# Performance work log

Measured on AMD Instinct MI355X. Metric: run time of the kernel, lower is better.

The kernel has to match this reference:

```python
import jax, jax.numpy as jnp
import numpy as np

HEADS = 8
DEPTH = 2
LN_EPS = 1e-5


def _layernorm(x, g, b):
    m = jnp.mean(x, axis=-1, keepdims=True)
    v = jnp.var(x, axis=-1, keepdims=True)
    return (x - m) / jnp.sqrt(v + LN_EPS) * g + b


def setup_inputs() -> dict:
    key = jax.random.key(0)
    ks = jax.random.split(key, 16)
    b, c, n, t = 4, 64, 512, 12
    L, H = DEPTH, 256  # depth, mlp_dim
    s = 0.05
    return {
        'x': jax.random.normal(ks[0], (b, c, n, t), jnp.float32),
        'adj': jax.random.uniform(ks[1], (n, n), jnp.float32) / n,
        'pos': 0.02 * jax.random.normal(ks[2], (1, n, c), jnp.float32),
        'qkv_w': s * jax.random.normal(ks[3], (L, 3 * c, c), jnp.float32),
        'proj_w': s * jax.random.normal(ks[4], (L, c, c), jnp.float32),
        'proj_b': jnp.zeros((L, c), jnp.float32),
        'ln_g': jnp.ones((L, c), jnp.float32),
        'ln_b': jnp.zeros((L, c), jnp.float32),
        'ff_w1': s * jax.random.normal(ks[5], (L, H, c), jnp.float32),
        'ff_b1': jnp.zeros((L, H), jnp.float32),
        'ff_w2': s * jax.random.normal(ks[6], (L, c, H), jnp.float32),
        'ff_b2': jnp.zeros((L, c), jnp.float32),
        'gcn_w': s * jax.random.normal(ks[7], (L, c, 3 * c), jnp.float32),  # Conv2d 1x1: [c_out, 3*c_in]
        'gcn_b': jnp.zeros((L, c), jnp.float32),
    }


def reference(x, adj, pos, qkv_w, proj_w, proj_b, ln_g, ln_b,
              ff_w1, ff_b1, ff_w2, ff_b2, gcn_w, gcn_b):
    b, c, n, t = x.shape
    hd = c // HEADS
    scale = hd ** (-0.5)
    # [b, c, n, t] -> [b*t, n, c]
    h = jnp.transpose(x, (0, 3, 2, 1)).reshape(b * t, n, c) + pos
    for l in range(DEPTH):
        residual = h.reshape(b, t, n, c)
        # --- manual MHA (no pre-norm around attention, faithful to source) ---
        qkv = jnp.einsum('bnc,oc->bno', h, qkv_w[l])  # [bt, n, 3c]
        qkv = qkv.reshape(b * t, n, 3, HEADS, hd).transpose(2, 0, 3, 1, 4)
        q, k, v = qkv[0], qkv[1], qkv[2]  # [bt, heads, n, hd]
        attn = jax.nn.softmax(jnp.einsum('bhnd,bhmd->bhnm', q, k) * scale, axis=-1)
        o = jnp.einsum('bhnm,bhmd->bhnd', attn, v)
        o = o.transpose(0, 2, 1, 3).reshape(b * t, n, c)
        o = jnp.einsum('bnc,oc->bno', o, proj_w[l]) + proj_b[l]
        h = o + h
        # --- PreNorm FeedForward ---
        y = _layernorm(h, ln_g[l], ln_b[l])
        y = jax.nn.gelu(jnp.einsum('bnc,hc->bnh', y, ff_w1[l]) + ff_b1[l], approximate=False)
        y = jnp.einsum('bnh,ch->bnc', y, ff_w2[l]) + ff_b2[l]
        h = y + h
        # --- GCN on residual (order=2 diffusion) ---
        r = jnp.transpose(residual, (0, 3, 2, 1))  # [b, c, n, t]
        x1 = jnp.einsum('bcvt,vw->bcwt', r, adj)
        x2 = jnp.einsum('bcvt,vw->bcwt', x1, adj)
        cat = jnp.concatenate([r, x1, x2], axis=1)  # [b, 3c, n, t]
        g = jnp.einsum('bknt,ok->bont', cat, gcn_w[l]) + gcn_b[l][None, :, None, None]
        h = jnp.transpose(g, (0, 3, 2, 1)).reshape(b * t, n, c) + h
    return jnp.transpose(h.reshape(b, t, n, c), (0, 3, 2, 1))
```

## Files before the change

### kernel.cpp

```cpp
#include <hip/hip_runtime.h>
#include <math.h>


typedef __fp16 half_t;
typedef __attribute__((ext_vector_type(2))) __fp16 half2v;
typedef __attribute__((ext_vector_type(4))) __fp16 half4v;
typedef __attribute__((ext_vector_type(4))) float f32x4;

union PU  { half2v h2[2]; half4v h4; };
union F4H { float4 f; half4v h[2]; };
union F2H { float2 f2; half4v h4; };

__global__ __launch_bounds__(256) void k_init(const float* __restrict__ x,
                                              const float* __restrict__ pos,
                                              float* __restrict__ h) {
    int i = blockIdx.x * 256 + threadIdx.x;
    int c = i & 63;
    int v = (i >> 6) & 511;
    int bt = i >> 15;
    int b = bt / 12, t = bt - b * 12;
    h[i] = x[(((size_t)(b * 64 + c) * 512) + v) * 12 + t] + pos[v * 64 + c];
}

__global__ __launch_bounds__(256) void k_prep(const float* __restrict__ qkv_w,
                                              const float* __restrict__ proj_w,
                                              const float* __restrict__ ff_w1,
                                              const float* __restrict__ ff_w2,
                                              const float* __restrict__ gcn_w,
                                              half_t* __restrict__ dst) {
    int i = blockIdx.x * 256 + threadIdx.x;
    float v;
    if (i < 24576) v = qkv_w[i];
    else if (i < 32768) v = proj_w[i - 24576];
    else if (i < 65536) v = ff_w1[i - 32768];
    else if (i < 98304) v = ff_w2[i - 65536];
    else v = gcn_w[i - 98304];
    dst[i] = (half_t)v;
}

__global__ __launch_bounds__(256) void k_adjt(const float* __restrict__ adj,
                                              half_t* __restrict__ adjTh) {
    __shared__ float t[64 * 65];
    int tid = threadIdx.x;
    int v0 = blockIdx.x * 64, w0 = blockIdx.y * 64;
#pragma unroll
    for (int i = 0; i < 4; ++i) {
        int g = tid + i * 256;
        int r = g >> 4, q = g & 15;
        float4 a = *(const float4*)(adj + (size_t)(v0 + r) * 512 + w0 + 4 * q);
        t[(4 * q + 0) * 65 + r] = a.x;
        t[(4 * q + 1) * 65 + r] = a.y;
        t[(4 * q + 2) * 65 + r] = a.z;
        t[(4 * q + 3) * 65 + r] = a.w;
    }
    __syncthreads();
#pragma unroll
    for (int i = 0; i < 4; ++i) {
        int g = tid + i * 256;
        int rw = g >> 4, q = g & 15;
        const float* src = &t[rw * 65 + 4 * q];
        PU u;
        u.h2[0] = __builtin_amdgcn_cvt_pkrtz(src[0], src[1]);
        u.h2[1] = __builtin_amdgcn_cvt_pkrtz(src[2], src[3]);
        *(half4v*)(adjTh + (size_t)(w0 + rw) * 512 + v0 + 4 * q) = u.h4;
    }
}

#define ATS 72
#define BTS 68

__global__ __launch_bounds__(256) void k_adj2(const half_t* __restrict__ adjTh,
                                              half_t* __restrict__ adjT2h) {
    __shared__ half_t a_t[64 * ATS];
    __shared__ half_t b_t[64 * BTS];
    int tid = threadIdx.x;
    int wave = tid >> 6, lane = tid & 63;
    int lm = lane & 15, lg = lane >> 4;
    int w0 = blockIdx.x * 64, v0 = blockIdx.y * 64;
    const f32x4 zc = {0.f, 0.f, 0.f, 0.f};
    f32x4 acc[4] = {zc, zc, zc, zc};

    for (int kc = 0; kc < 8; ++kc) {
#pragma unroll
        for (int i = 0; i < 2; ++i) {
            int g = tid + i * 256;
            int r = g >> 3, s = g & 7;
            *(float4*)&a_t[r * ATS + s * 8] =
                *(const float4*)(adjTh + (size_t)(w0 + r) * 512 + kc * 64 + s * 8);
        }
#pragma unroll
        for (int i = 0; i < 2; ++i) {
            int g = tid + i * 256;
            int ur = g >> 3, s = g & 7;
            F4H u;
            u.f = *(const float4*)(adjTh + (size_t)(kc * 64 + ur) * 512 + v0 + s * 8);
#pragma unroll
            for (int e = 0; e < 8; ++e)
                b_t[(s * 8 + e) * BTS + ur] = u.h[e >> 2][e & 3];
        }
        __syncthreads();
#pragma unroll
        for (int k16 = 0; k16 < 4; ++k16) {
            half4v af = *(const half4v*)&a_t[(wave * 16 + lm) * ATS + k16 * 16 + lg * 4];
#pragma unroll
            for (int nt = 0; nt < 4; ++nt) {
                half4v bf = *(const half4v*)&b_t[(nt * 16 + lm) * BTS + k16 * 16 + lg * 4];
                acc[nt] = __builtin_amdgcn_mfma_f32_16x16x16f16(af, bf, acc[nt], 0, 0, 0);
            }
        }
        __syncthreads();
    }
#pragma unroll
    for (int nt = 0; nt < 4; ++nt)
#pragma unroll
        for (int r = 0; r < 4; ++r)
            adjT2h[(size_t)(w0 + wave * 16 + lg * 4 + r) * 512 + v0 + nt * 16 + lm] =
                (half_t)acc[nt][r];
}

__global__ __launch_bounds__(128) void k_qkv(const float* __restrict__ h,
                                             const half_t* __restrict__ Wh,
                                             half_t* __restrict__ qh,
                                             half_t* __restrict__ kh,
                                             half_t* __restrict__ vh) {
    int wid = blockIdx.x * 2 + (threadIdx.x >> 6);
    int lane = threadIdx.x & 63;
    int lm = lane & 15, lg = lane >> 4;
    int row = wid * 16 + lm;

    half4v xf[4];
#pragma unroll
    for (int kc = 0; kc < 4; ++kc) {
        float4 a = *(const float4*)(h + (size_t)row * 64 + kc * 16 + lg * 4);
        PU u;
        u.h2[0] = __builtin_amdgcn_cvt_pkrtz(a.x, a.y);
        u.h2[1] = __builtin_amdgcn_cvt_pkrtz(a.z, a.w);
        xf[kc] = u.h4;
    }

    const f32x4 zc = {0.f, 0.f, 0.f, 0.f};
    const float SC = 0.35355339059327373f * 1.4426950408889634f;
    int bt = row >> 9, v = row & 511;

    half4v wf[4];
#pragma unroll
    for (int kc = 0; kc < 4; ++kc)
        wf[kc] = *(const half4v*)(Wh + (size_t)lm * 64 + kc * 16 + lg * 4);

#pragma unroll
    for (int nt = 0; nt < 12; ++nt) {
        half4v cw[4];
#pragma unroll
        for (int kc = 0; kc < 4; ++kc) cw[kc] = wf[kc];
        if (nt < 11) {
#pragma unroll
            for (int kc = 0; kc < 4; ++kc)
                wf[kc] = *(const half4v*)(Wh + (size_t)((nt + 1) * 16 + lm) * 64 + kc * 16 + lg * 4);
        }
        f32x4 acc = zc;
#pragma unroll
        for (int kc = 0; kc < 4; ++kc)
            acc = __builtin_amdgcn_mfma_f32_16x16x16f16(cw[kc], xf[kc], acc, 0, 0, 0);
        int s = nt >> 2;
        if (s == 0) { acc[0] *= SC; acc[1] *= SC; acc[2] *= SC; acc[3] *= SC; }
        int head = ((nt & 3) << 1) + (lg >> 1);
        int d0 = (lg & 1) * 4;
        PU o2;
        o2.h2[0] = __builtin_amdgcn_cvt_pkrtz(acc[0], acc[1]);
        o2.h2[1] = __builtin_amdgcn_cvt_pkrtz(acc[2], acc[3]);
        half_t* dst = (s == 0) ? qh : ((s == 1) ? kh : vh);
        *(half4v*)(dst + ((size_t)(bt * 8 + head) * 512 + v) * 8 + d0) = o2.h4;
    }
}

#define KLS 20
#define QLS 20
#define VTS 516

__global__ __launch_bounds__(512) void k_attn(const half_t* __restrict__ qh,
                                              const half_t* __restrict__ kh,
                                              const half_t* __restrict__ vh,
                                              half_t* __restrict__ obh) {
    __shared__ half_t kl[512 * KLS];
    __shared__ half_t vt[16 * VTS];
    __shared__ half_t ql[256 * QLS];
    int bh = blockIdx.x >> 1;
    int half_ = blockIdx.x & 1;
    int tid = threadIdx.x;
    const half_t* kbase = kh + (size_t)bh * 4096;
    const half_t* vbase = vh + (size_t)bh * 4096;
    const half_t* qbase = qh + (size_t)bh * 4096 + half_ * 2048;
    const half4v zero4 = {(__fp16)0.f, (__fp16)0.f, (__fp16)0.f, (__fp16)0.f};

    if (tid < 256) {
#pragma unroll
        for (int kk = 0; kk < 2; ++kk) {
            int key = tid * 2 + kk;
            F4H u;
            u.f = *(const float4*)(kbase + key * 8);
            half4v* rowp = (half4v*)&kl[key * KLS];
            rowp[0] = u.h[0];
            rowp[1] = u.h[1];
            rowp[2] = zero4;
            rowp[3] = zero4;
        }
        {
            F4H u;
            u.f = *(const float4*)(qbase + tid * 8);
            half4v* rowp = (half4v*)&ql[tid * QLS];
            rowp[0] = u.h[0];
            rowp[1] = u.h[1];
            rowp[2] = zero4;
            rowp[3] = zero4;
        }
        {
            int k0 = tid * 2;
            F4H a, b;
            a.f = *(const float4*)(vbase + k0 * 8);
            b.f = *(const float4*)(vbase + k0 * 8 + 8);
#pragma unroll
            for (int d = 0; d < 8; ++d) {
                half2v p = {a.h[d >> 2][d & 3], b.h[d >> 2][d & 3]};
                *(half2v*)&vt[d * VTS + k0] = p;
            }
        }
    }
    for (int i = tid; i < 1032; i += 512)
        ((half4v*)(vt + 8 * VTS))[i] = zero4;
    __syncthreads();

    int wave = tid >> 6, lane = tid & 63;
    int lm = lane & 15, lg = lane >> 4;
    int bt = bh >> 3, head = bh & 7;

#pragma unroll 1
    for (int st = 0; st < 2; ++st) {
        int qrow0 = wave * 32 + st * 16;
        half4v qf = *(const half4v*)&ql[(qrow0 + lm) * QLS + lg * 4];
        f32x4 acc = {0.f, 0.f, 0.f, 0.f};
        float l0 = 0.f, l1 = 0.f, l2 = 0.f, l3 = 0.f;
        f32x4 zc = {0.f, 0.f, 0.f, 0.f};
#pragma unroll 4
        for (int kt = 0; kt < 32; ++kt) {
            int key0 = kt * 16;
            half4v ka = *(const half4v*)&kl[(key0 + lm) * KLS + lg * 4];
            f32x4 c1 = __builtin_amdgcn_mfma_f32_16x16x16f16(ka, qf, zc, 0, 0, 0);
            float p0 = exp2f(fminf(c1[0], 12.f));
            float p1 = exp2f(fminf(c1[1], 12.f));
            float p2 = exp2f(fminf(c1[2], 12.f));
            float p3 = exp2f(fminf(c1[3], 12.f));
            l0 += p0; l1 += p1; l2 += p2; l3 += p3;
            PU pu;
            pu.h2[0] = __builtin_amdgcn_cvt_pkrtz(p0, p1);
            pu.h2[1] = __builtin_amdgcn_cvt_pkrtz(p2, p3);
            half4v va = *(const half4v*)&vt[lm * VTS + key0 + lg * 4];
            acc = __builtin_amdgcn_mfma_f32_16x16x16f16(va, pu.h4, acc, 0, 0, 0);
        }
        float lsum = (l0 + l1) + (l2 + l3);
        lsum += __shfl_xor(lsum, 16);
        lsum += __shfl_xor(lsum, 32);
        if (lg < 2) {
            float inv = 1.f / lsum;
            int rowg = half_ * 256 + qrow0 + lm;
            PU o2;
            o2.h2[0] = __builtin_amdgcn_cvt_pkrtz(acc[0] * inv, acc[1] * inv);
            o2.h2[1] = __builtin_amdgcn_cvt_pkrtz(acc[2] * inv, acc[3] * inv);
            *(half4v*)(obh + ((size_t)(bt * 512 + rowg)) * 64 + head * 8 + lg * 4) = o2.h4;
        }
    }
}

__global__ __launch_bounds__(256) void k_diffx2(const half_t* __restrict__ adjTh,
                                                const half_t* __restrict__ adjT2h,
                                                const float* __restrict__ h,
                                                half_t* __restrict__ x1h,
                                                half_t* __restrict__ x2h) {
    __shared__ half_t a_t[64 * ATS];
    __shared__ half_t b_t[64 * BTS];
    int tid = threadIdx.x;
    int wave = tid >> 6, lane = tid & 63;
    int lm = lane & 15, lg = lane >> 4;
    int w0 = blockIdx.x * 64;
    int bt = blockIdx.y;
    const half_t* A = blockIdx.z ? adjT2h : adjTh;
    half_t* outb = blockIdx.z ? x2h : x1h;
    const f32x4 zc = {0.f, 0.f, 0.f, 0.f};
    f32x4 acc[4] = {zc, zc, zc, zc};

    for (int kc = 0; kc < 8; ++kc) {
#pragma unroll
        for (int i = 0; i < 2; ++i) {
            int g = tid + i * 256;
            int r = g >> 3, s = g & 7;
            *(float4*)&a_t[r * ATS + s * 8] =
                *(const float4*)(A + (size_t)(w0 + r) * 512 + kc * 64 + s * 8);
        }
#pragma unroll
        for (int i = 0; i < 4; ++i) {
            int g = tid + i * 256;
            int vr = g >> 4, q = g & 15;
            float4 a = *(const float4*)(h + ((size_t)(bt * 512 + kc * 64 + vr)) * 64 + 4 * q);
            b_t[(4 * q + 0) * BTS + vr] = (half_t)a.x;
            b_t[(4 * q + 1) * BTS + vr] = (half_t)a.y;
            b_t[(4 * q + 2) * BTS + vr] = (half_t)a.z;
            b_t[(4 * q + 3) * BTS + vr] = (half_t)a.w;
        }
        __syncthreads();
#pragma unroll
        for (int k16 = 0; k16 < 4; ++k16) {
            half4v af = *(const half4v*)&a_t[(wave * 16 + lm) * ATS + k16 * 16 + lg * 4];
#pragma unroll
            for (int nt = 0; nt < 4; ++nt) {
                half4v bf = *(const half4v*)&b_t[(nt * 16 + lm) * BTS + k16 * 16 + lg * 4];
                acc[nt] = __builtin_amdgcn_mfma_f32_16x16x16f16(af, bf, acc[nt], 0, 0, 0);
            }
        }
        __syncthreads();
    }
#pragma unroll
    for (int nt = 0; nt < 4; ++nt)
#pragma unroll
        for (int r = 0; r < 4; ++r)
            outb[(size_t)(w0 + wave * 16 + lg * 4 + r) * 3072 + bt * 64 + nt * 16 + lm] =
                (half_t)acc[nt][r];
}

__global__ __launch_bounds__(256) void k_gcn(const float* __restrict__ h,
                                             const half_t* __restrict__ x1h,
                                             const half_t* __restrict__ x2h,
                                             const half_t* __restrict__ Wh,
                                             const float* __restrict__ bias,
                                             float* __restrict__ gout) {
    __shared__ half_t a_t[64 * ATS];
    __shared__ half_t b_t[64 * BTS];
    int tid = threadIdx.x;
    int wave = tid >> 6, lane = tid & 63;
    int lm = lane & 15, lg = lane >> 4;
    int row0 = blockIdx.x * 64;
    const f32x4 zc = {0.f, 0.f, 0.f, 0.f};
    f32x4 acc[4] = {zc, zc, zc, zc};

    for (int ch = 0; ch < 3; ++ch) {
        if (ch == 0) {
#pragma unroll
            for (int i = 0; i < 4; ++i) {
                int g = tid + i * 256;
                int r = g >> 4, q = g & 15;
                int rowg = row0 + r;
                int v = rowg / 48, bt = rowg - v * 48;
                float4 a = *(const float4*)(h + ((size_t)(bt * 512 + v)) * 64 + 4 * q);
                PU ua;
                ua.h2[0] = __builtin_amdgcn_cvt_pkrtz(a.x, a.y);
                ua.h2[1] = __builtin_amdgcn_cvt_pkrtz(a.z, a.w);
                *(half4v*)&a_t[r * ATS + 4 * q] = ua.h4;
            }
        } else {
            const half_t* X = (ch == 1) ? x1h : x2h;
#pragma unroll
            for (int i = 0; i < 2; ++i) {
                int g = tid + i * 256;
                int r = g >> 3, s = g & 7;
                *(float4*)&a_t[r * ATS + s * 8] =
                    *(const float4*)(X + (size_t)(row0 + r) * 64 + s * 8);
            }
        }
#pragma unroll
        for (int i = 0; i < 4; ++i) {
            int g = tid + i * 256;
            int r = g >> 4, q = g & 15;
            *(half4v*)&b_t[r * BTS + 4 * q] =
                *(const half4v*)(Wh + (size_t)r * 192 + ch * 64 + 4 * q);
        }
        __syncthreads();
#pragma unroll
        for (int k16 = 0; k16 < 4; ++k16) {
            half4v af = *(const half4v*)&a_t[(wave * 16 + lm) * ATS + k16 * 16 + lg * 4];
#pragma unroll
            for (int nt = 0; nt < 4; ++nt) {
                half4v bf = *(const half4v*)&b_t[(nt * 16 + lm) * BTS + k16 * 16 + lg * 4];
                acc[nt] = __builtin_amdgcn_mfma_f32_16x16x16f16(bf, af, acc[nt], 0, 0, 0);
            }
        }
        __syncthreads();
    }
    int row = row0 + wave * 16 + lm;
    int v = row / 48, bt = row - v * 48;
    float* gp = gout + ((size_t)(bt * 512 + v)) * 64;
#pragma unroll
    for (int nt = 0; nt < 4; ++nt) {
        float4 bb = *(const float4*)(bias + nt * 16 + lg * 4);
        *(float4*)(gp + nt * 16 + lg * 4) =
            make_float4(acc[nt][0] + bb.x, acc[nt][1] + bb.y,
                        acc[nt][2] + bb.z, acc[nt][3] + bb.w);
    }
}

__global__ __launch_bounds__(128) void k_plf(const half_t* __restrict__ obh,
                                             const half_t* __restrict__ pwh,
                                             const float* __restrict__ pb,
                                             const float* __restrict__ g,
                                             const float* __restrict__ bln,
                                             const half_t* __restrict__ w1h,
                                             const float* __restrict__ b1,
                                             const half_t* __restrict__ w2h,
                                             const float* __restrict__ b2,
                                             const float* __restrict__ gout,
                                             float* __restrict__ h) {
    int wid = blockIdx.x * 2 + (threadIdx.x >> 6);
    int lane = threadIdx.x & 63;
    int lm = lane & 15, lg = lane >> 4;
    int row = wid * 16 + lm;
    const f32x4 zc = {0.f, 0.f, 0.f, 0.f};

    half4v pf[4];
#pragma unroll
    for (int kc = 0; kc < 4; ++kc)
        pf[kc] = *(const half4v*)(pwh + (size_t)lm * 64 + kc * 16 + lg * 4);

    half4v of[4];
#pragma unroll
    for (int kc = 0; kc < 4; ++kc) {
        F2H u;
        u.f2 = *(const float2*)(obh + (size_t)row * 64 + kc * 16 + lg * 4);
        of[kc] = u.h4;
    }

    f32x4 hp[4];
#pragma unroll
    for (int nt = 0; nt < 4; ++nt) {
        half4v cw[4];
#pragma unroll
        for (int kc = 0; kc < 4; ++kc) cw[kc] = pf[kc];
        if (nt < 3) {
#pragma unroll
            for (int kc = 0; kc < 4; ++kc)
                pf[kc] = *(const half4v*)(pwh + (size_t)((nt + 1) * 16 + lm) * 64 + kc * 16 + lg * 4);
        }
        f32x4 c = zc;
#pragma unroll
        for (int kc = 0; kc < 4; ++kc)
            c = __builtin_amdgcn_mfma_f32_16x16x16f16(cw[kc], of[kc], c, 0, 0, 0);
        float4 ho = *(const float4*)(h + (size_t)row * 64 + nt * 16 + lg * 4);
        float4 bb = *(const float4*)(pb + nt * 16 + lg * 4);
        hp[nt][0] = c[0] + ho.x + bb.x;
        hp[nt][1] = c[1] + ho.y + bb.y;
        hp[nt][2] = c[2] + ho.z + bb.z;
        hp[nt][3] = c[3] + ho.w + bb.w;
    }

    float s = 0.f, s2 = 0.f;
#pragma unroll
    for (int nt = 0; nt < 4; ++nt)
#pragma unroll
        for (int r = 0; r < 4; ++r) {
            s += hp[nt][r];
            s2 += hp[nt][r] * hp[nt][r];
        }
    s += __shfl_xor(s, 16);  s2 += __shfl_xor(s2, 16);
    s += __shfl_xor(s, 32);  s2 += __shfl_xor(s2, 32);
    float mean = s * (1.f / 64.f);
    float var = s2 * (1.f / 64.f) - mean * mean;
    float rstd = rsqrtf(var + 1e-5f);

    half4v xf[4];
#pragma unroll
    for (int nt = 0; nt < 4; ++nt) {
        float4 gg = *(const float4*)(g + nt * 16 + lg * 4);
        float4 bb = *(const float4*)(bln + nt * 16 + lg * 4);
        float y0 = (hp[nt][0] - mean) * rstd * gg.x + bb.x;
        float y1 = (hp[nt][1] - mean) * rstd * gg.y + bb.y;
        float y2 = (hp[nt][2] - mean) * rstd * gg.z + bb.z;
        float y3 = (hp[nt][3] - mean) * rstd * gg.w + bb.w;
        PU u;
        u.h2[0] = __builtin_amdgcn_cvt_pkrtz(y0, y1);
        u.h2[1] = __builtin_amdgcn_cvt_pkrtz(y2, y3);
        xf[nt] = u.h4;
    }

    half4v w1f[4];
#pragma unroll
    for (int kc = 0; kc < 4; ++kc)
        w1f[kc] = *(const half4v*)(w1h + (size_t)lm * 64 + kc * 16 + lg * 4);

    f32x4 acc[4] = {zc, zc, zc, zc};
#pragma unroll 4
    for (int ht = 0; ht < 16; ++ht) {
        half4v cw[4];
#pragma unroll
        for (int kc = 0; kc < 4; ++kc) cw[kc] = w1f[kc];
        half4v w2f[4];
#pragma unroll
        for (int ot = 0; ot < 4; ++ot)
            w2f[ot] = *(const half4v*)(w2h + (size_t)(ot * 16 + lm) * 256 + ht * 16 + lg * 4);
        if (ht < 15) {
#pragma unroll
            for (int kc = 0; kc < 4; ++kc)
                w1f[kc] = *(const half4v*)(w1h + (size_t)((ht + 1) * 16 + lm) * 64 + kc * 16 + lg * 4);
        }
        f32x4 c1 = zc;
#pragma unroll
        for (int kc = 0; kc < 4; ++kc)
            c1 = __builtin_amdgcn_mfma_f32_16x16x16f16(cw[kc], xf[kc], c1, 0, 0, 0);
        float4 bb = *(const float4*)(b1 + ht * 16 + lg * 4);
        float y0 = c1[0] + bb.x;
        float y1 = c1[1] + bb.y;
        float y2 = c1[2] + bb.z;
        float y3 = c1[3] + bb.w;
        y0 = 0.5f * y0 * (1.0f + erff(y0 * 0.70710678118654752f));
        y1 = 0.5f * y1 * (1.0f + erff(y1 * 0.70710678118654752f));
        y2 = 0.5f * y2 * (1.0f + erff(y2 * 0.70710678118654752f));
        y3 = 0.5f * y3 * (1.0f + erff(y3 * 0.70710678118654752f));
        PU p;
        p.h2[0] = __builtin_amdgcn_cvt_pkrtz(y0, y1);
        p.h2[1] = __builtin_amdgcn_cvt_pkrtz(y2, y3);
#pragma unroll
        for (int ot = 0; ot < 4; ++ot)
            acc[ot] = __builtin_amdgcn_mfma_f32_16x16x16f16(w2f[ot], p.h4, acc[ot], 0, 0, 0);
    }

#pragma unroll
    for (int ot = 0; ot < 4; ++ot) {
        float4 bb = *(const float4*)(b2 + ot * 16 + lg * 4);
        float4 gv = *(const float4*)(gout + (size_t)row * 64 + ot * 16 + lg * 4);
        *(float4*)(h + (size_t)row * 64 + ot * 16 + lg * 4) =
            make_float4(hp[ot][0] + acc[ot][0] + bb.x + gv.x,
                        hp[ot][1] + acc[ot][1] + bb.y + gv.y,
                        hp[ot][2] + acc[ot][2] + bb.z + gv.z,
                        hp[ot][3] + acc[ot][3] + bb.w + gv.w);
    }
}

__global__ __launch_bounds__(256) void k_out(const float* __restrict__ h,
                                             float* __restrict__ out) {
    int i = blockIdx.x * 256 + threadIdx.x;
    int t = i % 12;
    int r = i / 12;
    int v = r & 511;
    int r2 = r >> 9;
    int c = r2 & 63;
    int b = r2 >> 6;
    out[i] = h[(((size_t)(b * 12 + t) * 512) + v) * 64 + c];
}

extern "C" void kernel_launch(void* const* d_in, const int* in_sizes, int n_in,
                              void* d_out, int out_size, void* d_ws, size_t ws_size,
                              hipStream_t stream) {
    const float* x      = (const float*)d_in[0];
    const float* adj    = (const float*)d_in[1];
    const float* pos    = (const float*)d_in[2];
    const float* qkv_w  = (const float*)d_in[3];
    const float* proj_w = (const float*)d_in[4];
    const float* proj_b = (const float*)d_in[5];
    const float* ln_g   = (const float*)d_in[6];
    const float* ln_b   = (const float*)d_in[7];
    const float* ff_w1  = (const float*)d_in[8];
    const float* ff_b1  = (const float*)d_in[9];
    const float* ff_w2  = (const float*)d_in[10];
    const float* ff_b2  = (const float*)d_in[11];
    const float* gcn_w  = (const float*)d_in[12];
    const float* gcn_b  = (const float*)d_in[13];
    float* out = (float*)d_out;

    const size_t SZ = 1572864;
    float* h    = (float*)d_ws;
    float* gout = h + SZ;
    half_t* x1h = (half_t*)(gout + SZ);
    half_t* x2h = x1h + SZ;
    half_t* qh  = x2h + SZ;
    half_t* kh  = qh + SZ;
    half_t* vh  = kh + SZ;
    half_t* obh = vh + SZ;
    half_t* adjTh  = obh + SZ;
    half_t* adjT2h = adjTh + 262144;
    half_t* wh     = adjT2h + 262144;
    half_t* qkv_wh  = wh;
    half_t* proj_wh = wh + 24576;
    half_t* ff_w1h  = wh + 32768;
    half_t* ff_w2h  = wh + 65536;
    half_t* gcn_wh  = wh + 98304;

    k_init<<<6144, 256, 0, stream>>>(x, pos, h);
    k_adjt<<<dim3(8, 8), 256, 0, stream>>>(adj, adjTh);
    k_prep<<<480, 256, 0, stream>>>(qkv_w, proj_w, ff_w1, ff_w2, gcn_w, wh);
    k_adj2<<<dim3(8, 8), 256, 0, stream>>>(adjTh, adjT2h);
    for (int l = 0; l < 2; ++l) {
        k_qkv<<<768, 128, 0, stream>>>(h, qkv_wh + l * 12288, qh, kh, vh);
        k_attn<<<768, 512, 0, stream>>>(qh, kh, vh, obh);
        k_diffx2<<<dim3(8, 48, 2), 256, 0, stream>>>(adjTh, adjT2h, h, x1h, x2h);
        k_gcn<<<384, 256, 0, stream>>>(h, x1h, x2h, gcn_wh + l * 12288, gcn_b + l * 64, gout);
        k_plf<<<768, 128, 0, stream>>>(obh, proj_wh + l * 4096, proj_b + l * 64,
                                       ln_g + l * 64, ln_b + l * 64,
                                       ff_w1h + l * 16384, ff_b1 + l * 256,
                                       ff_w2h + l * 16384, ff_b2 + l * 64, gout, h);
    }
    k_out<<<6144, 256, 0, stream>>>(h, out);
}
```

Baseline: 320.6 us.

## Merge independent kernels via block-index dispatch and tile init/out transposes

Merges the prep kernels (input transpose, adj transpose, weight conversion) into one launch, runs QKV projection together with the adjacency diffusion in one launch, and runs attention together with the GCN channel mix in another, each role picked by block index. Independent stages can then overlap on the GPU and there are fewer launches per layer. The init and output permutes now go through shared-memory tiles so global accesses coalesce. The cost is heterogeneous blocks: the GCN part runs at 512 threads with half of them idle, and the fused kernels must size their shared memory for the larger role.

```diff
diff --git a/kernel.cpp b/kernel.cpp
--- a/kernel.cpp
+++ b/kernel.cpp
@@ -11,63 +11,85 @@
 union F4H { float4 f; half4v h[2]; };
 union F2H { float2 f2; half4v h4; };
 
-__global__ __launch_bounds__(256) void k_init(const float* __restrict__ x,
-                                              const float* __restrict__ pos,
-                                              float* __restrict__ h) {
-    int i = blockIdx.x * 256 + threadIdx.x;
-    int c = i & 63;
-    int v = (i >> 6) & 511;
-    int bt = i >> 15;
-    int b = bt / 12, t = bt - b * 12;
-    h[i] = x[(((size_t)(b * 64 + c) * 512) + v) * 12 + t] + pos[v * 64 + c];
-}
-
-__global__ __launch_bounds__(256) void k_prep(const float* __restrict__ qkv_w,
-                                              const float* __restrict__ proj_w,
-                                              const float* __restrict__ ff_w1,
-                                              const float* __restrict__ ff_w2,
-                                              const float* __restrict__ gcn_w,
-                                              half_t* __restrict__ dst) {
-    int i = blockIdx.x * 256 + threadIdx.x;
-    float v;
-    if (i < 24576) v = qkv_w[i];
-    else if (i < 32768) v = proj_w[i - 24576];
-    else if (i < 65536) v = ff_w1[i - 32768];
-    else if (i < 98304) v = ff_w2[i - 65536];
-    else v = gcn_w[i - 98304];
-    dst[i] = (half_t)v;
-}
-
-__global__ __launch_bounds__(256) void k_adjt(const float* __restrict__ adj,
-                                              half_t* __restrict__ adjTh) {
+#define ATS 72
+#define BTS 68
+#define KLS 20
+#define QLS 20
+#define VTS 516
+
+__global__ __launch_bounds__(256) void k_pre(const float* __restrict__ x,
+                                             const float* __restrict__ pos,
+                                             const float* __restrict__ adj,
+                                             const float* __restrict__ qkv_w,
+                                             const float* __restrict__ proj_w,
+                                             const float* __restrict__ ff_w1,
+                                             const float* __restrict__ ff_w2,
+                                             const float* __restrict__ gcn_w,
+                                             float* __restrict__ h,
+                                             half_t* __restrict__ adjTh,
+                                             half_t* __restrict__ wh) {
     __shared__ float t[64 * 65];
     int tid = threadIdx.x;
-    int v0 = blockIdx.x * 64, w0 = blockIdx.y * 64;
-#pragma unroll
-    for (int i = 0; i < 4; ++i) {
-        int g = tid + i * 256;
-        int r = g >> 4, q = g & 15;
-        float4 a = *(const float4*)(adj + (size_t)(v0 + r) * 512 + w0 + 4 * q);
-        t[(4 * q + 0) * 65 + r] = a.x;
-        t[(4 * q + 1) * 65 + r] = a.y;
-        t[(4 * q + 2) * 65 + r] = a.z;
-        t[(4 * q + 3) * 65 + r] = a.w;
-    }
-    __syncthreads();
-#pragma unroll
-    for (int i = 0; i < 4; ++i) {
-        int g = tid + i * 256;
-        int rw = g >> 4, q = g & 15;
-        const float* src = &t[rw * 65 + 4 * q];
-        PU u;
-        u.h2[0] = __builtin_amdgcn_cvt_pkrtz(src[0], src[1]);
-        u.h2[1] = __builtin_amdgcn_cvt_pkrtz(src[2], src[3]);
-        *(half4v*)(adjTh + (size_t)(w0 + rw) * 512 + v0 + 4 * q) = u.h4;
+    int bidx = blockIdx.x;
+    if (bidx < 384) {
+        int b = bidx / 96, vt0 = (bidx % 96) * 64;
+#pragma unroll
+        for (int i = 0; i < 4; ++i) {
+            int g = tid + i * 256;
+            int r = g >> 4, q = g & 15;
+            *(float4*)&t[r * 65 + 4 * q] =
+                *(const float4*)(x + ((size_t)(b * 64 + r)) * 6144 + vt0 + 4 * q);
+        }
+        __syncthreads();
+#pragma unroll
+        for (int i = 0; i < 4; ++i) {
+            int g = tid + i * 256;
+            int r = g >> 4, q = g & 15;
+            int vt = vt0 + r;
+            int v = vt / 12, tt = vt - v * 12;
+            float4 pv = *(const float4*)(pos + v * 64 + 4 * q);
+            float4 o;
+            o.x = t[(4 * q + 0) * 65 + r] + pv.x;
+            o.y = t[(4 * q + 1) * 65 + r] + pv.y;
+            o.z = t[(4 * q + 2) * 65 + r] + pv.z;
+            o.w = t[(4 * q + 3) * 65 + r] + pv.w;
+            *(float4*)(h + ((size_t)((b * 12 + tt) * 512 + v)) * 64 + 4 * q) = o;
+        }
+    } else if (bidx < 448) {
+        int fb = bidx - 384;
+        int v0 = (fb & 7) * 64, w0 = (fb >> 3) * 64;
+#pragma unroll
+        for (int i = 0; i < 4; ++i) {
+            int g = tid + i * 256;
+            int r = g >> 4, q = g & 15;
+            float4 a = *(const float4*)(adj + (size_t)(v0 + r) * 512 + w0 + 4 * q);
+            t[(4 * q + 0) * 65 + r] = a.x;
+            t[(4 * q + 1) * 65 + r] = a.y;
+            t[(4 * q + 2) * 65 + r] = a.z;
+            t[(4 * q + 3) * 65 + r] = a.w;
+        }
+        __syncthreads();
+#pragma unroll
+        for (int i = 0; i < 4; ++i) {
+            int g = tid + i * 256;
+            int rw = g >> 4, q = g & 15;
+            const float* src = &t[rw * 65 + 4 * q];
+            PU u;
+            u.h2[0] = __builtin_amdgcn_cvt_pkrtz(src[0], src[1]);
+            u.h2[1] = __builtin_amdgcn_cvt_pkrtz(src[2], src[3]);
+            *(half4v*)(adjTh + (size_t)(w0 + rw) * 512 + v0 + 4 * q) = u.h4;
+        }
+    } else {
+        int i = (bidx - 448) * 256 + tid;
+        float v;
+        if (i < 24576) v = qkv_w[i];
+        else if (i < 32768) v = proj_w[i - 24576];
+        else if (i < 65536) v = ff_w1[i - 32768];
+        else if (i < 98304) v = ff_w2[i - 65536];
+        else v = gcn_w[i - 98304];
+        wh[i] = (half_t)v;
     }
 }
-
-#define ATS 72
-#define BTS 68
 
 __global__ __launch_bounds__(256) void k_adj2(const half_t* __restrict__ adjTh,
                                               half_t* __restrict__ adjT2h) {
@@ -118,280 +140,281 @@
                 (half_t)acc[nt][r];
 }
 
-__global__ __launch_bounds__(128) void k_qkv(const float* __restrict__ h,
-                                             const half_t* __restrict__ Wh,
-                                             half_t* __restrict__ qh,
-                                             half_t* __restrict__ kh,
-                                             half_t* __restrict__ vh) {
-    int wid = blockIdx.x * 2 + (threadIdx.x >> 6);
-    int lane = threadIdx.x & 63;
-    int lm = lane & 15, lg = lane >> 4;
-    int row = wid * 16 + lm;
-
-    half4v xf[4];
-#pragma unroll
-    for (int kc = 0; kc < 4; ++kc) {
-        float4 a = *(const float4*)(h + (size_t)row * 64 + kc * 16 + lg * 4);
-        PU u;
-        u.h2[0] = __builtin_amdgcn_cvt_pkrtz(a.x, a.y);
-        u.h2[1] = __builtin_amdgcn_cvt_pkrtz(a.z, a.w);
-        xf[kc] = u.h4;
-    }
-
-    const f32x4 zc = {0.f, 0.f, 0.f, 0.f};
-    const float SC = 0.35355339059327373f * 1.4426950408889634f;
-    int bt = row >> 9, v = row & 511;
-
-    half4v wf[4];
-#pragma unroll
-    for (int kc = 0; kc < 4; ++kc)
-        wf[kc] = *(const half4v*)(Wh + (size_t)lm * 64 + kc * 16 + lg * 4);
-
-#pragma unroll
-    for (int nt = 0; nt < 12; ++nt) {
-        half4v cw[4];
-#pragma unroll
-        for (int kc = 0; kc < 4; ++kc) cw[kc] = wf[kc];
-        if (nt < 11) {
-#pragma unroll
-            for (int kc = 0; kc < 4; ++kc)
-                wf[kc] = *(const half4v*)(Wh + (size_t)((nt + 1) * 16 + lm) * 64 + kc * 16 + lg * 4);
-        }
-        f32x4 acc = zc;
-#pragma unroll
-        for (int kc = 0; kc < 4; ++kc)
-            acc = __builtin_amdgcn_mfma_f32_16x16x16f16(cw[kc], xf[kc], acc, 0, 0, 0);
-        int s = nt >> 2;
-        if (s == 0) { acc[0] *= SC; acc[1] *= SC; acc[2] *= SC; acc[3] *= SC; }
-        int head = ((nt & 3) << 1) + (lg >> 1);
-        int d0 = (lg & 1) * 4;
-        PU o2;
-        o2.h2[0] = __builtin_amdgcn_cvt_pkrtz(acc[0], acc[1]);
-        o2.h2[1] = __builtin_amdgcn_cvt_pkrtz(acc[2], acc[3]);
-        half_t* dst = (s == 0) ? qh : ((s == 1) ? kh : vh);
-        *(half4v*)(dst + ((size_t)(bt * 8 + head) * 512 + v) * 8 + d0) = o2.h4;
-    }
-}
-
-#define KLS 20
-#define QLS 20
-#define VTS 516
-
-__global__ __launch_bounds__(512) void k_attn(const half_t* __restrict__ qh,
-                                              const half_t* __restrict__ kh,
-                                              const half_t* __restrict__ vh,
-                                              half_t* __restrict__ obh) {
-    __shared__ half_t kl[512 * KLS];
-    __shared__ half_t vt[16 * VTS];
-    __shared__ half_t ql[256 * QLS];
-    int bh = blockIdx.x >> 1;
-    int half_ = blockIdx.x & 1;
+__global__ __launch_bounds__(256) void k_qd(const float* __restrict__ h,
+                                            const half_t* __restrict__ Wh,
+                                            half_t* __restrict__ qh,
+                                            half_t* __restrict__ kh,
+                                            half_t* __restrict__ vh,
+                                            const half_t* __restrict__ adjTh,
+                                            const half_t* __restrict__ adjT2h,
+                                            half_t* __restrict__ x1h,
+                                            half_t* __restrict__ x2h) {
+    __shared__ __align__(16) half_t sbuf[64 * ATS + 64 * BTS];
     int tid = threadIdx.x;
-    const half_t* kbase = kh + (size_t)bh * 4096;
-    const half_t* vbase = vh + (size_t)bh * 4096;
-    const half_t* qbase = qh + (size_t)bh * 4096 + half_ * 2048;
-    const half4v zero4 = {(__fp16)0.f, (__fp16)0.f, (__fp16)0.f, (__fp16)0.f};
-
-    if (tid < 256) {
-#pragma unroll
-        for (int kk = 0; kk < 2; ++kk) {
-            int key = tid * 2 + kk;
-            F4H u;
-            u.f = *(const float4*)(kbase + key * 8);
-            half4v* rowp = (half4v*)&kl[key * KLS];
-            rowp[0] = u.h[0];
-            rowp[1] = u.h[1];
-            rowp[2] = zero4;
-            rowp[3] = zero4;
-        }
-        {
-            F4H u;
-            u.f = *(const float4*)(qbase + tid * 8);
-            half4v* rowp = (half4v*)&ql[tid * QLS];
-            rowp[0] = u.h[0];
-            rowp[1] = u.h[1];
-            rowp[2] = zero4;
-            rowp[3] = zero4;
-        }
-        {
-            int k0 = tid * 2;
-            F4H a, b;
-            a.f = *(const float4*)(vbase + k0 * 8);
-            b.f = *(const float4*)(vbase + k0 * 8 + 8);
-#pragma unroll
-            for (int d = 0; d < 8; ++d) {
-                half2v p = {a.h[d >> 2][d & 3], b.h[d >> 2][d & 3]};
-                *(half2v*)&vt[d * VTS + k0] = p;
-            }
-        }
-    }
-    for (int i = tid; i < 1032; i += 512)
-        ((half4v*)(vt + 8 * VTS))[i] = zero4;
-    __syncthreads();
-
+    int bidx = blockIdx.x;
     int wave = tid >> 6, lane = tid & 63;
     int lm = lane & 15, lg = lane >> 4;
-    int bt = bh >> 3, head = bh & 7;
-
-#pragma unroll 1
-    for (int st = 0; st < 2; ++st) {
-        int qrow0 = wave * 32 + st * 16;
-        half4v qf = *(const half4v*)&ql[(qrow0 + lm) * QLS + lg * 4];
-        f32x4 acc = {0.f, 0.f, 0.f, 0.f};
-        float l0 = 0.f, l1 = 0.f, l2 = 0.f, l3 = 0.f;
-        f32x4 zc = {0.f, 0.f, 0.f, 0.f};
-#pragma unroll 4
-        for (int kt = 0; kt < 32; ++kt) {
-            int key0 = kt * 16;
-            half4v ka = *(const half4v*)&kl[(key0 + lm) * KLS + lg * 4];
-            f32x4 c1 = __builtin_amdgcn_mfma_f32_16x16x16f16(ka, qf, zc, 0, 0, 0);
-            float p0 = exp2f(fminf(c1[0], 12.f));
-            float p1 = exp2f(fminf(c1[1], 12.f));
-            float p2 = exp2f(fminf(c1[2], 12.f));
-            float p3 = exp2f(fminf(c1[3], 12.f));
-            l0 += p0; l1 += p1; l2 += p2; l3 += p3;
-            PU pu;
-            pu.h2[0] = __builtin_amdgcn_cvt_pkrtz(p0, p1);
-            pu.h2[1] = __builtin_amdgcn_cvt_pkrtz(p2, p3);
-            half4v va = *(const half4v*)&vt[lm * VTS + key0 + lg * 4];
-            acc = __builtin_amdgcn_mfma_f32_16x16x16f16(va, pu.h4, acc, 0, 0, 0);
-        }
-        float lsum = (l0 + l1) + (l2 + l3);
-        lsum += __shfl_xor(lsum, 16);
-        lsum += __shfl_xor(lsum, 32);
-        if (lg < 2) {
-            float inv = 1.f / lsum;
-            int rowg = half_ * 256 + qrow0 + lm;
+    const f32x4 zc = {0.f, 0.f, 0.f, 0.f};
+
+    if (bidx < 384) {
+        int wid = bidx * 4 + wave;
+        int row = wid * 16 + lm;
+        half4v xf[4];
+#pragma unroll
+        for (int kc = 0; kc < 4; ++kc) {
+            float4 a = *(const float4*)(h + (size_t)row * 64 + kc * 16 + lg * 4);
+            PU u;
+            u.h2[0] = __builtin_amdgcn_cvt_pkrtz(a.x, a.y);
+            u.h2[1] = __builtin_amdgcn_cvt_pkrtz(a.z, a.w);
+            xf[kc] = u.h4;
+        }
+        const float SC = 0.35355339059327373f * 1.4426950408889634f;
+        int bt = row >> 9, v = row & 511;
+        half4v wf[4];
+#pragma unroll
+        for (int kc = 0; kc < 4; ++kc)
+            wf[kc] = *(const half4v*)(Wh + (size_t)lm * 64 + kc * 16 + lg * 4);
+#pragma unroll
+        for (int nt = 0; nt < 12; ++nt) {
+            half4v cw[4];
+#pragma unroll
+            for (int kc = 0; kc < 4; ++kc) cw[kc] = wf[kc];
+            if (nt < 11) {
+#pragma unroll
+                for (int kc = 0; kc < 4; ++kc)
+                    wf[kc] = *(const half4v*)(Wh + (size_t)((nt + 1) * 16 + lm) * 64 + kc * 16 + lg * 4);
+            }
+            f32x4 acc = zc;
+#pragma unroll
+            for (int kc = 0; kc < 4; ++kc)
+                acc = __builtin_amdgcn_mfma_f32_16x16x16f16(cw[kc], xf[kc], acc, 0, 0, 0);
+            int s = nt >> 2;
+            if (s == 0) { acc[0] *= SC; acc[1] *= SC; acc[2] *= SC; acc[3] *= SC; }
+            int head = ((nt & 3) << 1) + (lg >> 1);
+            int d0 = (lg & 1) * 4;
             PU o2;
-            o2.h2[0] = __builtin_amdgcn_cvt_pkrtz(acc[0] * inv, acc[1] * inv);
-            o2.h2[1] = __builtin_amdgcn_cvt_pkrtz(acc[2] * inv, acc[3] * inv);
-            *(half4v*)(obh + ((size_t)(bt * 512 + rowg)) * 64 + head * 8 + lg * 4) = o2.h4;
-        }
-    }
-}
-
-__global__ __launch_bounds__(256) void k_diffx2(const half_t* __restrict__ adjTh,
-                                                const half_t* __restrict__ adjT2h,
-                                                const float* __restrict__ h,
-                                                half_t* __restrict__ x1h,
-                                                half_t* __restrict__ x2h) {
-    __shared__ half_t a_t[64 * ATS];
-    __shared__ half_t b_t[64 * BTS];
-    int tid = threadIdx.x;
-    int wave = tid >> 6, lane = tid & 63;
-    int lm = lane & 15, lg = lane >> 4;
-    int w0 = blockIdx.x * 64;
-    int bt = blockIdx.y;
-    const half_t* A = blockIdx.z ? adjT2h : adjTh;
-    half_t* outb = blockIdx.z ? x2h : x1h;
-    const f32x4 zc = {0.f, 0.f, 0.f, 0.f};
-    f32x4 acc[4] = {zc, zc, zc, zc};
-
-    for (int kc = 0; kc < 8; ++kc) {
-#pragma unroll
-        for (int i = 0; i < 2; ++i) {
-            int g = tid + i * 256;
-            int r = g >> 3, s = g & 7;
-            *(float4*)&a_t[r * ATS + s * 8] =
-                *(const float4*)(A + (size_t)(w0 + r) * 512 + kc * 64 + s * 8);
-        }
-#pragma unroll
-        for (int i = 0; i < 4; ++i) {
-            int g = tid + i * 256;
-            int vr = g >> 4, q = g & 15;
-            float4 a = *(const float4*)(h + ((size_t)(bt * 512 + kc * 64 + vr)) * 64 + 4 * q);
-            b_t[(4 * q + 0) * BTS + vr] = (half_t)a.x;
-            b_t[(4 * q + 1) * BTS + vr] = (half_t)a.y;
-            b_t[(4 * q + 2) * BTS + vr] = (half_t)a.z;
-            b_t[(4 * q + 3) * BTS + vr] = (half_t)a.w;
-        }
-        __syncthreads();
-#pragma unroll
-        for (int k16 = 0; k16 < 4; ++k16) {
-            half4v af = *(const half4v*)&a_t[(wave * 16 + lm) * ATS + k16 * 16 + lg * 4];
-#pragma unroll
-            for (int nt = 0; nt < 4; ++nt) {
-                half4v bf = *(const half4v*)&b_t[(nt * 16 + lm) * BTS + k16 * 16 + lg * 4];
-                acc[nt] = __builtin_amdgcn_mfma_f32_16x16x16f16(af, bf, acc[nt], 0, 0, 0);
-            }
-        }
-        __syncthreads();
-    }
-#pragma unroll
-    for (int nt = 0; nt < 4; ++nt)
-#pragma unroll
-        for (int r = 0; r < 4; ++r)
-            outb[(size_t)(w0 + wave * 16 + lg * 4 + r) * 3072 + bt * 64 + nt * 16 + lm] =
-                (half_t)acc[nt][r];
-}
-
-__global__ __launch_bounds__(256) void k_gcn(const float* __restrict__ h,
-                                             const half_t* __restrict__ x1h,
-                                             const half_t* __restrict__ x2h,
-                                             const half_t* __restrict__ Wh,
-                                             const float* __restrict__ bias,
-                                             float* __restrict__ gout) {
-    __shared__ half_t a_t[64 * ATS];
-    __shared__ half_t b_t[64 * BTS];
-    int tid = threadIdx.x;
-    int wave = tid >> 6, lane = tid & 63;
-    int lm = lane & 15, lg = lane >> 4;
-    int row0 = blockIdx.x * 64;
-    const f32x4 zc = {0.f, 0.f, 0.f, 0.f};
-    f32x4 acc[4] = {zc, zc, zc, zc};
-
-    for (int ch = 0; ch < 3; ++ch) {
-        if (ch == 0) {
-#pragma unroll
-            for (int i = 0; i < 4; ++i) {
-                int g = tid + i * 256;
-                int r = g >> 4, q = g & 15;
-                int rowg = row0 + r;
-                int v = rowg / 48, bt = rowg - v * 48;
-                float4 a = *(const float4*)(h + ((size_t)(bt * 512 + v)) * 64 + 4 * q);
-                PU ua;
-                ua.h2[0] = __builtin_amdgcn_cvt_pkrtz(a.x, a.y);
-                ua.h2[1] = __builtin_amdgcn_cvt_pkrtz(a.z, a.w);
-                *(half4v*)&a_t[r * ATS + 4 * q] = ua.h4;
-            }
-        } else {
-            const half_t* X = (ch == 1) ? x1h : x2h;
+            o2.h2[0] = __builtin_amdgcn_cvt_pkrtz(acc[0], acc[1]);
+            o2.h2[1] = __builtin_amdgcn_cvt_pkrtz(acc[2], acc[3]);
+            half_t* dst = (s == 0) ? qh : ((s == 1) ? kh : vh);
+            *(half4v*)(dst + ((size_t)(bt * 8 + head) * 512 + v) * 8 + d0) = o2.h4;
+        }
+    } else {
+        half_t* a_t = sbuf;
+        half_t* b_t = sbuf + 64 * ATS;
+        int fb = bidx - 384;
+        int z = fb / 384, rem = fb - z * 384;
+        int w0 = (rem & 7) * 64;
+        int bt = rem >> 3;
+        const half_t* A = z ? adjT2h : adjTh;
+        half_t* outb = z ? x2h : x1h;
+        f32x4 acc[4] = {zc, zc, zc, zc};
+        for (int kc = 0; kc < 8; ++kc) {
 #pragma unroll
             for (int i = 0; i < 2; ++i) {
                 int g = tid + i * 256;
                 int r = g >> 3, s = g & 7;
                 *(float4*)&a_t[r * ATS + s * 8] =
-                    *(const float4*)(X + (size_t)(row0 + r) * 64 + s * 8);
-            }
-        }
-#pragma unroll
-        for (int i = 0; i < 4; ++i) {
-            int g = tid + i * 256;
-            int r = g >> 4, q = g & 15;
-            *(half4v*)&b_t[r * BTS + 4 * q] =
-                *(const half4v*)(Wh + (size_t)r * 192 + ch * 64 + 4 * q);
-        }
+                    *(const float4*)(A + (size_t)(w0 + r) * 512 + kc * 64 + s * 8);
+            }
+#pragma unroll
+            for (int i = 0; i < 4; ++i) {
+                int g = tid + i * 256;
+                int vr = g >> 4, q = g & 15;
+                float4 a = *(const float4*)(h + ((size_t)(bt * 512 + kc * 64 + vr)) * 64 + 4 * q);
+                b_t[(4 * q + 0) * BTS + vr] = (half_t)a.x;
+                b_t[(4 * q + 1) * BTS + vr] = (half_t)a.y;
+                b_t[(4 * q + 2) * BTS + vr] = (half_t)a.z;
+                b_t[(4 * q + 3) * BTS + vr] = (half_t)a.w;
+            }
+            __syncthreads();
+#pragma unroll
+            for (int k16 = 0; k16 < 4; ++k16) {
+                half4v af = *(const half4v*)&a_t[(wave * 16 + lm) * ATS + k16 * 16 + lg * 4];
+#pragma unroll
+                for (int nt = 0; nt < 4; ++nt) {
+                    half4v bf = *(const half4v*)&b_t[(nt * 16 + lm) * BTS + k16 * 16 + lg * 4];
+                    acc[nt] = __builtin_amdgcn_mfma_f32_16x16x16f16(af, bf, acc[nt], 0, 0, 0);
+                }
+            }
+            __syncthreads();
+        }
+#pragma unroll
+        for (int nt = 0; nt < 4; ++nt)
+#pragma unroll
+            for (int r = 0; r < 4; ++r)
+                outb[(size_t)(w0 + wave * 16 + lg * 4 + r) * 3072 + bt * 64 + nt * 16 + lm] =
+                    (half_t)acc[nt][r];
+    }
+}
+
+__global__ __launch_bounds__(512) void k_ag(const half_t* __restrict__ qh,
+                                            const half_t* __restrict__ kh,
+                                            const half_t* __restrict__ vh,
+                                            half_t* __restrict__ obh,
+                                            const float* __restrict__ h,
+                                            const half_t* __restrict__ x1h,
+                                            const half_t* __restrict__ x2h,
+                                            const half_t* __restrict__ Wh,
+                                            const float* __restrict__ bias,
+                                            float* __restrict__ gout) {
+    __shared__ __align__(16) half_t sbuf[512 * KLS + 16 * VTS + 256 * QLS];
+    int tid = threadIdx.x;
+    int bidx = blockIdx.x;
+    const half4v zero4 = {(__fp16)0.f, (__fp16)0.f, (__fp16)0.f, (__fp16)0.f};
+    const f32x4 zc = {0.f, 0.f, 0.f, 0.f};
+
+    if (bidx < 768) {
+        half_t* kl = sbuf;
+        half_t* vt = sbuf + 512 * KLS;
+        half_t* ql = sbuf + 512 * KLS + 16 * VTS;
+        int bh = bidx >> 1;
+        int half_ = bidx & 1;
+        const half_t* kbase = kh + (size_t)bh * 4096;
+        const half_t* vbase = vh + (size_t)bh * 4096;
+        const half_t* qbase = qh + (size_t)bh * 4096 + half_ * 2048;
+
+        if (tid < 256) {
+#pragma unroll
+            for (int kk = 0; kk < 2; ++kk) {
+                int key = tid * 2 + kk;
+                F4H u;
+                u.f = *(const float4*)(kbase + key * 8);
+                half4v* rowp = (half4v*)&kl[key * KLS];
+                rowp[0] = u.h[0];
+                rowp[1] = u.h[1];
+                rowp[2] = zero4;
+                rowp[3] = zero4;
+            }
+            {
+                F4H u;
+                u.f = *(const float4*)(qbase + tid * 8);
+                half4v* rowp = (half4v*)&ql[tid * QLS];
+                rowp[0] = u.h[0];
+                rowp[1] = u.h[1];
+                rowp[2] = zero4;
+                rowp[3] = zero4;
+            }
+            {
+                int k0 = tid * 2;
+                F4H a, b;
+                a.f = *(const float4*)(vbase + k0 * 8);
+                b.f = *(const float4*)(vbase + k0 * 8 + 8);
+#pragma unroll
+                for (int d = 0; d < 8; ++d) {
+                    half2v p = {a.h[d >> 2][d & 3], b.h[d >> 2][d & 3]};
+                    *(half2v*)&vt[d * VTS + k0] = p;
+                }
+            }
+        }
+        for (int i = tid; i < 1032; i += 512)
+            ((half4v*)(vt + 8 * VTS))[i] = zero4;
         __syncthreads();
-#pragma unroll
-        for (int k16 = 0; k16 < 4; ++k16) {
-            half4v af = *(const half4v*)&a_t[(wave * 16 + lm) * ATS + k16 * 16 + lg * 4];
+
+        int wave = tid >> 6, lane = tid & 63;
+        int lm = lane & 15, lg = lane >> 4;
+        int bt = bh >> 3, head = bh & 7;
+
+#pragma unroll 1
+        for (int st = 0; st < 2; ++st) {
+            int qrow0 = wave * 32 + st * 16;
+            half4v qf = *(const half4v*)&ql[(qrow0 + lm) * QLS + lg * 4];
+            f32x4 acc = zc;
+            float l0 = 0.f, l1 = 0.f, l2 = 0.f, l3 = 0.f;
+#pragma unroll 4
+            for (int kt = 0; kt < 32; ++kt) {
+                int key0 = kt * 16;
+                half4v ka = *(const half4v*)&kl[(key0 + lm) * KLS + lg * 4];
+                f32x4 c1 = __builtin_amdgcn_mfma_f32_16x16x16f16(ka, qf, zc, 0, 0, 0);
+                float p0 = exp2f(fminf(c1[0], 12.f));
+                float p1 = exp2f(fminf(c1[1], 12.f));
+                float p2 = exp2f(fminf(c1[2], 12.f));
+                float p3 = exp2f(fminf(c1[3], 12.f));
+                l0 += p0; l1 += p1; l2 += p2; l3 += p3;
+                PU pu;
+                pu.h2[0] = __builtin_amdgcn_cvt_pkrtz(p0, p1);
+                pu.h2[1] = __builtin_amdgcn_cvt_pkrtz(p2, p3);
+                half4v va = *(const half4v*)&vt[lm * VTS + key0 + lg * 4];
+                acc = __builtin_amdgcn_mfma_f32_16x16x16f16(va, pu.h4, acc, 0, 0, 0);
+            }
+            float lsum = (l0 + l1) + (l2 + l3);
+            lsum += __shfl_xor(lsum, 16);
+            lsum += __shfl_xor(lsum, 32);
+            if (lg < 2) {
+                float inv = 1.f / lsum;
+                int rowg = half_ * 256 + qrow0 + lm;
+                PU o2;
+                o2.h2[0] = __builtin_amdgcn_cvt_pkrtz(acc[0] * inv, acc[1] * inv);
+                o2.h2[1] = __builtin_amdgcn_cvt_pkrtz(acc[2] * inv, acc[3] * inv);
+                *(half4v*)(obh + ((size_t)(bt * 512 + rowg)) * 64 + head * 8 + lg * 4) = o2.h4;
+            }
+        }
+    } else {
+        half_t* a_t = sbuf;
+        half_t* b_t = sbuf + 64 * ATS;
+        int row0 = (bidx - 768) * 64;
+        int wave = tid >> 6, lane = tid & 63;
+        int lm = lane & 15, lg = lane >> 4;
+        f32x4 acc[4] = {zc, zc, zc, zc};
+
+        for (int ch = 0; ch < 3; ++ch) {
+            if (tid < 256) {
+                if (ch == 0) {
+#pragma unroll
+                    for (int i = 0; i < 4; ++i) {
+                        int g = tid + i * 256;
+                        int r = g >> 4, q = g & 15;
+                        int rowg = row0 + r;
+                        int v = rowg / 48, bt = rowg - v * 48;
+                        float4 a = *(const float4*)(h + ((size_t)(bt * 512 + v)) * 64 + 4 * q);
+                        PU ua;
+                        ua.h2[0] = __builtin_amdgcn_cvt_pkrtz(a.x, a.y);
+                        ua.h2[1] = __builtin_amdgcn_cvt_pkrtz(a.z, a.w);
+                        *(half4v*)&a_t[r * ATS + 4 * q] = ua.h4;
+                    }
+                } else {
+                    const half_t* X = (ch == 1) ? x1h : x2h;
+#pragma unroll
+                    for (int i = 0; i < 2; ++i) {
+                        int g = tid + i * 256;
+                        int r = g >> 3, s = g & 7;
+                        *(float4*)&a_t[r * ATS + s * 8] =
+                            *(const float4*)(X + (size_t)(row0 + r) * 64 + s * 8);
+                    }
+                }
+#pragma unroll
+                for (int i = 0; i < 4; ++i) {
+                    int g = tid + i * 256;
+                    int r = g >> 4, q = g & 15;
+                    *(half4v*)&b_t[r * BTS + 4 * q] =
+                        *(const half4v*)(Wh + (size_t)r * 192 + ch * 64 + 4 * q);
+                }
+            }
+            __syncthreads();
+            if (tid < 256) {
+#pragma unroll
+                for (int k16 = 0; k16 < 4; ++k16) {
+                    half4v af = *(const half4v*)&a_t[(wave * 16 + lm) * ATS + k16 * 16 + lg * 4];
+#pragma unroll
+                    for (int nt = 0; nt < 4; ++nt) {
+                        half4v bf = *(const half4v*)&b_t[(nt * 16 + lm) * BTS + k16 * 16 + lg * 4];
+                        acc[nt] = __builtin_amdgcn_mfma_f32_16x16x16f16(bf, af, acc[nt], 0, 0, 0);
+                    }
+                }
+            }
+            __syncthreads();
+        }
+        if (tid < 256) {
+            int row = row0 + wave * 16 + lm;
+            int v = row / 48, bt = row - v * 48;
+            float* gp = gout + ((size_t)(bt * 512 + v)) * 64;
 #pragma unroll
             for (int nt = 0; nt < 4; ++nt) {
-                half4v bf = *(const half4v*)&b_t[(nt * 16 + lm) * BTS + k16 * 16 + lg * 4];
-                acc[nt] = __builtin_amdgcn_mfma_f32_16x16x16f16(bf, af, acc[nt], 0, 0, 0);
-            }
-        }
-        __syncthreads();
-    }
-    int row = row0 + wave * 16 + lm;
-    int v = row / 48, bt = row - v * 48;
-    float* gp = gout + ((size_t)(bt * 512 + v)) * 64;
-#pragma unroll
-    for (int nt = 0; nt < 4; ++nt) {
-        float4 bb = *(const float4*)(bias + nt * 16 + lg * 4);
-        *(float4*)(gp + nt * 16 + lg * 4) =
-            make_float4(acc[nt][0] + bb.x, acc[nt][1] + bb.y,
-                        acc[nt][2] + bb.z, acc[nt][3] + bb.w);
+                float4 bb = *(const float4*)(bias + nt * 16 + lg * 4);
+                *(float4*)(gp + nt * 16 + lg * 4) =
+                    make_float4(acc[nt][0] + bb.x, acc[nt][1] + bb.y,
+                                acc[nt][2] + bb.z, acc[nt][3] + bb.w);
+            }
+        }
     }
 }
 
@@ -532,14 +555,30 @@
 
 __global__ __launch_bounds__(256) void k_out(const float* __restrict__ h,
                                              float* __restrict__ out) {
-    int i = blockIdx.x * 256 + threadIdx.x;
-    int t = i % 12;
-    int r = i / 12;
-    int v = r & 511;
-    int r2 = r >> 9;
-    int c = r2 & 63;
-    int b = r2 >> 6;
-    out[i] = h[(((size_t)(b * 12 + t) * 512) + v) * 64 + c];
+    __shared__ float t[64 * 65];
+    int tid = threadIdx.x;
+    int b = blockIdx.x / 96, vt0 = (blockIdx.x % 96) * 64;
+#pragma unroll
+    for (int i = 0; i < 4; ++i) {
+        int g = tid + i * 256;
+        int r = g >> 4, q = g & 15;
+        int vt = vt0 + r;
+        int v = vt / 12, tt = vt - v * 12;
+        *(float4*)&t[r * 65 + 4 * q] =
+            *(const float4*)(h + ((size_t)((b * 12 + tt) * 512 + v)) * 64 + 4 * q);
+    }
+    __syncthreads();
+#pragma unroll
+    for (int i = 0; i < 4; ++i) {
+        int g = tid + i * 256;
+        int r = g >> 4, q = g & 15;
+        float4 o;
+        o.x = t[(4 * q + 0) * 65 + r];
+        o.y = t[(4 * q + 1) * 65 + r];
+        o.z = t[(4 * q + 2) * 65 + r];
+        o.w = t[(4 * q + 3) * 65 + r];
+        *(float4*)(out + ((size_t)(b * 64 + r)) * 6144 + vt0 + 4 * q) = o;
+    }
 }
 
 extern "C" void kernel_launch(void* const* d_in, const int* in_sizes, int n_in,
@@ -579,19 +618,18 @@
     half_t* ff_w2h  = wh + 65536;
     half_t* gcn_wh  = wh + 98304;
 
-    k_init<<<6144, 256, 0, stream>>>(x, pos, h);
-    k_adjt<<<dim3(8, 8), 256, 0, stream>>>(adj, adjTh);
-    k_prep<<<480, 256, 0, stream>>>(qkv_w, proj_w, ff_w1, ff_w2, gcn_w, wh);
+    k_pre<<<928, 256, 0, stream>>>(x, pos, adj, qkv_w, proj_w, ff_w1, ff_w2, gcn_w,
+                                   h, adjTh, wh);
     k_adj2<<<dim3(8, 8), 256, 0, stream>>>(adjTh, adjT2h);
     for (int l = 0; l < 2; ++l) {
-        k_qkv<<<768, 128, 0, stream>>>(h, qkv_wh + l * 12288, qh, kh, vh);
-        k_attn<<<768, 512, 0, stream>>>(qh, kh, vh, obh);
-        k_diffx2<<<dim3(8, 48, 2), 256, 0, stream>>>(adjTh, adjT2h, h, x1h, x2h);
-        k_gcn<<<384, 256, 0, stream>>>(h, x1h, x2h, gcn_wh + l * 12288, gcn_b + l * 64, gout);
+        k_qd<<<1152, 256, 0, stream>>>(h, qkv_wh + l * 12288, qh, kh, vh,
+                                       adjTh, adjT2h, x1h, x2h);
+        k_ag<<<1152, 512, 0, stream>>>(qh, kh, vh, obh, h, x1h, x2h,
+                                       gcn_wh + l * 12288, gcn_b + l * 64, gout);
         k_plf<<<768, 128, 0, stream>>>(obh, proj_wh + l * 4096, proj_b + l * 64,
                                        ln_g + l * 64, ln_b + l * 64,
                                        ff_w1h + l * 16384, ff_b1 + l * 256,
                                        ff_w2h + l * 16384, ff_b2 + l * 64, gout, h);
     }
-    k_out<<<6144, 256, 0, stream>>>(h, out);
+    k_out<<<384, 256, 0, stream>>>(h, out);
 }
```

New measurement: 288.0 us. -10.2%, faster.
